# Kernel tuning notes

Measured on AMD Instinct MI355X. Metric: run time of the kernel, lower is better.

## Reference

```python
import jax, jax.numpy as jnp
import numpy as np

KUP = 5       # reassembly kernel size
DELTA = 2     # upsample ratio
KENC = 3      # encoder conv kernel size
CM = 64       # compressed channels
INC = 256
OUTC = 256


def conv2d(x, w, b, pad):
    # x: (N,C,H,W), w: (O,I,kh,kw)
    y = jax.lax.conv_general_dilated(
        x, w, window_strides=(1, 1), padding=[(pad, pad), (pad, pad)],
        dimension_numbers=("NCHW", "OIHW", "NCHW"))
    return y + b[None, :, None, None]


def pixel_shuffle(x, r):
    # torch semantics: channel c*r^2 + i*r + j -> (c, h*r+i, w*r+j)
    N, Cr2, H, W = x.shape
    C = Cr2 // (r * r)
    x = x.reshape(N, C, r, r, H, W)
    x = x.transpose(0, 1, 4, 2, 5, 3)
    return x.reshape(N, C, H * r, W * r)


def setup_inputs() -> dict:
    key = jax.random.key(0)
    ks = jax.random.split(key, 7)
    N, H, W = 4, 64, 64
    x = jax.random.normal(ks[0], (N, INC, H, W), dtype=jnp.float32)
    w_down = jax.random.normal(ks[1], (CM, INC, 1, 1), dtype=jnp.float32) * 0.05
    b_down = jnp.zeros((CM,), jnp.float32)
    enc_out = DELTA * DELTA * KUP * KUP  # 100
    w_enc = jax.random.normal(ks[2], (enc_out, CM, KENC, KENC), dtype=jnp.float32) * 0.05
    b_enc = jnp.zeros((enc_out,), jnp.float32)
    w_out = jax.random.normal(ks[3], (OUTC, INC, 1, 1), dtype=jnp.float32) * 0.05
    b_out = jnp.zeros((OUTC,), jnp.float32)
    return {"in_tensor": x, "w_down": w_down, "b_down": b_down,
            "w_enc": w_enc, "b_enc": b_enc, "w_out": w_out, "b_out": b_out}


def reference(in_tensor, w_down, b_down, w_enc, b_enc, w_out, b_out):
    N, C, H, W = in_tensor.shape
    k2, d2 = KUP * KUP, DELTA * DELTA

    # --- kernel prediction branch ---
    k = conv2d(in_tensor, w_down, b_down, 0)          # (N, Cm, H, W)
    k = conv2d(k, w_enc, b_enc, KENC // 2)            # (N, k2*d2, H, W)
    # pixel_shuffle + per-upsampled-pixel softmax over Kup^2, fused:
    # channel index = kup_idx * delta^2 + subpixel_idx (torch pixel_shuffle layout)
    k = k.reshape(N, k2, d2, H, W)
    k = jax.nn.softmax(k, axis=1)
    kern = k.transpose(0, 3, 4, 1, 2)                 # (N, H, W, k2, d2)

    # --- feature reassembly ---
    pad = KUP // 2
    xp = jnp.pad(in_tensor, ((0, 0), (0, 0), (pad, pad), (pad, pad)))
    # (N, C, H, W, Kup^2); k index = kh*Kup + kw, matching torch unfold order
    patches = jnp.stack(
        [xp[:, :, i:i + H, j:j + W] for i in range(KUP) for j in range(KUP)],
        axis=-1)

    out = jnp.einsum("nchwk,nhwkd->nhwcd", patches, kern)  # (N,H,W,C,d2)
    out = out.reshape(N, H, W, C * d2).transpose(0, 3, 1, 2)  # (N, C*d2, H, W)
    out = pixel_shuffle(out, DELTA)                   # (N, C, H*delta, W*delta)

    return conv2d(out, w_out, b_out, 0)               # (N, outC, H*delta, W*delta)
```

## Files before the change

kernel.cpp:

```cpp
#include <hip/hip_runtime.h>
#include <hip/hip_bf16.h>


namespace {
constexpr int kN = 4, kH = 64, kW = 64, kINC = 256, kCM = 64;
constexpr int kENC = 100, kH2 = 128, kW2 = 128, kOUTC = 256;
constexpr int kHW = kH * kW;
constexpr int kHW2 = kH2 * kW2;
constexpr int kPadW = 66;
constexpr int kTImg = kPadW * kPadW * kCM;
constexpr int kZPad = 68;
constexpr int kZImg = kZPad * kZPad * kOUTC;
}

typedef __attribute__((ext_vector_type(8))) short short8;
typedef __attribute__((ext_vector_type(4))) float floatx4;

static __device__ __forceinline__ unsigned short bf16bits(float f) {
  __hip_bfloat16 h = __float2bfloat16(f);
  return *(unsigned short*)&h;
}

__global__ __launch_bounds__(256) void k_repack(
    const float* __restrict__ we, unsigned short* __restrict__ Aswz) {
  const int e = blockIdx.x * 256 + threadIdx.x;
  if (e >= 9 * 7 * 2 * 512) return;
  const int j = e & 7, lane = (e >> 3) & 63, kh = (e >> 9) & 1, tm = e >> 10;
  const int mt = tm % 7, tap = tm / 7;
  const int o = mt * 16 + (lane & 15);
  const int ci = kh * 32 + ((lane >> 4) & 3) * 8 + j;
  const float v = (o < kENC) ? we[(size_t)o * 576 + ci * 9 + tap] : 0.f;
  Aswz[e] = bf16bits(v);
}

__global__ __launch_bounds__(256) void k_repack_woz(
    const float* __restrict__ wd, const float* __restrict__ wo,
    unsigned short* __restrict__ Awoz) {
  const int e = blockIdx.x * 256 + threadIdx.x;
  if (e >= 8 * 20 * 512) return;
  const int j = e & 7, lane = (e >> 3) & 63;
  const int rest = e >> 9;
  const int mt = rest % 20, ks = rest / 20;
  const int r = mt * 16 + (lane & 15);
  const int k = ks * 32 + (lane >> 4) * 8 + j;
  const float v = (r < kCM) ? wd[(size_t)r * kINC + k]
                            : wo[(size_t)(r - kCM) * kINC + k];
  Awoz[e] = bf16bits(v);
}

__global__ __launch_bounds__(256) void k_dzmfma(
    const float* __restrict__ x, const unsigned short* __restrict__ Awoz,
    const float* __restrict__ bd, __hip_bfloat16* __restrict__ downT,
    float* __restrict__ zT) {
  const int b = blockIdx.x;
  const int pt = b & 255, n = b >> 8;
  const int wave = threadIdx.x >> 6, lane = threadIdx.x & 63;
  const int col = lane & 15, quad = lane >> 4;
  const int px = pt * 16 + col;
  const int h = px >> 6, w = px & 63;
  const float* xb = x + (size_t)n * kINC * kHW + px;

  floatx4 acc[5];
#pragma unroll
  for (int m = 0; m < 5; ++m) acc[m] = (floatx4){0.f, 0.f, 0.f, 0.f};

#pragma unroll
  for (int ks = 0; ks < 8; ++ks) {
    float xv[8];
#pragma unroll
    for (int j = 0; j < 8; ++j)
      xv[j] = xb[(size_t)(ks * 32 + quad * 8 + j) * kHW];
    short8 bf;
#pragma unroll
    for (int j = 0; j < 8; ++j) bf[j] = (short)bf16bits(xv[j]);
#pragma unroll
    for (int m = 0; m < 5; ++m) {
      const int wtile = wave * 5 + m;
      const short8 af = *(const short8*)(
          Awoz + ((size_t)(ks * 20 + wtile) * 64 + lane) * 8);
      acc[m] = __builtin_amdgcn_mfma_f32_16x16x32_bf16(af, bf, acc[m], 0, 0, 0);
    }
  }

#pragma unroll
  for (int m = 0; m < 5; ++m) {
    const int wtile = wave * 5 + m;
    const int r0 = wtile * 16 + quad * 4;
    if (wtile < 4) {
      union { unsigned short u[4]; uint2 v; } pk;
#pragma unroll
      for (int rr = 0; rr < 4; ++rr)
        pk.u[rr] = bf16bits(acc[m][rr] + bd[r0 + rr]);
      __hip_bfloat16* dst = downT + (size_t)n * kTImg
                            + ((h + 1) * kPadW + (w + 1)) * kCM + r0;
      *(uint2*)dst = pk.v;
    } else {
      const int o = r0 - kCM;
      float* dst = zT + (size_t)n * kZImg
                   + ((h + 2) * kZPad + (w + 2)) * kOUTC + o;
      *(float4*)dst = make_float4(acc[m][0], acc[m][1], acc[m][2], acc[m][3]);
    }
  }
}

__global__ __launch_bounds__(256) void k_encmfma(
    const __hip_bfloat16* __restrict__ downT,
    const unsigned short* __restrict__ Aswz,
    const float* __restrict__ be, float* __restrict__ enc) {
  const int b = blockIdx.x;
  const int h = b & 63, mtp = (b >> 6) & 3, n = b >> 8;
  const int wave = threadIdx.x >> 6, lane = threadIdx.x & 63;
  const int w0 = wave << 4;
  const int col = lane & 15, quad = lane >> 4;
  const int mt0 = mtp * 2;
  const bool has2 = (mt0 + 1) < 7;
  const short* dT = (const short*)downT + (size_t)n * kTImg;
  floatx4 acc0 = {0.f, 0.f, 0.f, 0.f}, acc1 = {0.f, 0.f, 0.f, 0.f};
#pragma unroll
  for (int tap = 0; tap < 9; ++tap) {
    const int dh = tap / 3 - 1, dw = tap % 3 - 1;
    const int rowbase = ((h + 1 + dh) * kPadW + (w0 + col + 1 + dw)) * kCM
                        + quad * 8;
#pragma unroll
    for (int kh = 0; kh < 2; ++kh) {
      const short8 bf = *(const short8*)(dT + rowbase + kh * 32);
      const short8 a0 = *(const short8*)(
          Aswz + (((size_t)(tap * 7 + mt0) * 2 + kh) * 64 + lane) * 8);
      acc0 = __builtin_amdgcn_mfma_f32_16x16x32_bf16(a0, bf, acc0, 0, 0, 0);
      if (has2) {
        const short8 a1 = *(const short8*)(
            Aswz + (((size_t)(tap * 7 + mt0 + 1) * 2 + kh) * 64 + lane) * 8);
        acc1 = __builtin_amdgcn_mfma_f32_16x16x32_bf16(a1, bf, acc1, 0, 0, 0);
      }
    }
  }
  const int p = h * kW + w0 + col;
#pragma unroll
  for (int r = 0; r < 4; ++r) {
    const int o = mt0 * 16 + quad * 4 + r;
    if (o < kENC) enc[(size_t)(n * kENC + o) * kHW + p] = acc0[r] + be[o];
  }
  if (has2) {
#pragma unroll
    for (int r = 0; r < 4; ++r) {
      const int o = (mt0 + 1) * 16 + quad * 4 + r;
      if (o < kENC) enc[(size_t)(n * kENC + o) * kHW + p] = acc1[r] + be[o];
    }
  }
}

__global__ __launch_bounds__(64) void k_softmaxT(
    const float* __restrict__ enc, float* __restrict__ kernT) {
  const int t = blockIdx.x * 64 + threadIdx.x;
  const int n = t >> 12, px = t & 4095;
  const float* base = enc + (size_t)n * kENC * kHW + px;
  float v[100];
#pragma unroll
  for (int ch = 0; ch < 100; ++ch) v[ch] = base[(size_t)ch * kHW];
  float inv[4];
#pragma unroll
  for (int d = 0; d < 4; ++d) {
    float m = -1e30f;
#pragma unroll
    for (int k = 0; k < 25; ++k) m = fmaxf(m, v[k * 4 + d]);
    float s = 0.f;
#pragma unroll
    for (int k = 0; k < 25; ++k) { v[k * 4 + d] = __expf(v[k * 4 + d] - m); s += v[k * 4 + d]; }
    inv[d] = 1.f / s;
  }
  float* dst = kernT + ((size_t)n * kHW + px) * 100;
#pragma unroll
  for (int k = 0; k < 25; ++k)
    *(float4*)(dst + k * 4) = make_float4(v[k * 4 + 0] * inv[0], v[k * 4 + 1] * inv[1],
                                          v[k * 4 + 2] * inv[2], v[k * 4 + 3] * inv[3]);
}

__global__ __launch_bounds__(256) void k_fused_out(
    const float* __restrict__ zT, const float* __restrict__ kernT,
    const float* __restrict__ bo, float* __restrict__ out) {
  const int b = blockIdx.x;
  const int pt = b & 255, ob = (b >> 8) & 3, n = b >> 10;
  const int wave = threadIdx.x >> 6, lane = threadIdx.x & 63;
  const int oc = lane & 15, pxi = lane >> 4;
  const int px = pt * 16 + wave * 4 + pxi;
  const int h = px >> 6, w = px & 63;
  const int o = ob * 64 + oc * 4;
  const float* kb = kernT + ((size_t)n * kHW + px) * 100;
  const float* zb = zT + (size_t)n * kZImg + o;
  float acc[4][4] = {};
#pragma unroll
  for (int tap = 0; tap < 25; ++tap) {
    const int kh = tap / 5 - 2, kw = tap % 5 - 2;
    const float4 kf = *(const float4*)(kb + tap * 4);
    const float4 zf = *(const float4*)(
        zb + ((size_t)(h + 2 + kh) * kZPad + (w + 2 + kw)) * kOUTC);
    acc[0][0] += zf.x * kf.x; acc[0][1] += zf.x * kf.y; acc[0][2] += zf.x * kf.z; acc[0][3] += zf.x * kf.w;
    acc[1][0] += zf.y * kf.x; acc[1][1] += zf.y * kf.y; acc[1][2] += zf.y * kf.z; acc[1][3] += zf.y * kf.w;
    acc[2][0] += zf.z * kf.x; acc[2][1] += zf.z * kf.y; acc[2][2] += zf.z * kf.z; acc[2][3] += zf.z * kf.w;
    acc[3][0] += zf.w * kf.x; acc[3][1] += zf.w * kf.y; acc[3][2] += zf.w * kf.z; acc[3][3] += zf.w * kf.w;
  }
#pragma unroll
  for (int oi = 0; oi < 4; ++oi) {
    const float bias = bo[o + oi];
#pragma unroll
    for (int i = 0; i < 2; ++i) {
      float* dst = out + ((size_t)(n * kOUTC + o + oi) * kH2 + (2 * h + i)) * kW2 + 2 * w;
      *(float2*)dst = make_float2(acc[oi][i * 2] + bias, acc[oi][i * 2 + 1] + bias);
    }
  }
}

extern "C" void kernel_launch(void* const* d_in, const int* in_sizes, int n_in,
                              void* d_out, int out_size, void* d_ws, size_t ws_size,
                              hipStream_t stream) {
  const float* x  = (const float*)d_in[0];
  const float* wd = (const float*)d_in[1];
  const float* bd = (const float*)d_in[2];
  const float* we = (const float*)d_in[3];
  const float* be = (const float*)d_in[4];
  const float* wo = (const float*)d_in[5];
  const float* bo = (const float*)d_in[6];
  float* out = (float*)d_out;

  float* enc   = (float*)d_ws;
  float* kernT = enc + 1638400;
  float* zT    = kernT + 1638400;
  __hip_bfloat16* downT = (__hip_bfloat16*)(zT + 4734976);
  unsigned short* Aswz  = (unsigned short*)(downT + (size_t)kN * kTImg);
  unsigned short* Awoz  = Aswz + 64512;

  hipMemsetAsync(downT, 0, (size_t)kN * kTImg * sizeof(__hip_bfloat16), stream);
  hipMemsetAsync(zT, 0, (size_t)kN * kZImg * sizeof(float), stream);
  k_repack<<<252, 256, 0, stream>>>(we, Aswz);
  k_repack_woz<<<320, 256, 0, stream>>>(wd, wo, Awoz);
  k_dzmfma<<<1024, 256, 0, stream>>>(x, Awoz, bd, downT, zT);
  k_encmfma<<<1024, 256, 0, stream>>>(downT, Aswz, be, enc);
  k_softmaxT<<<256, 64, 0, stream>>>(enc, kernT);
  k_fused_out<<<4096, 256, 0, stream>>>(zT, kernT, bo, out);
}
```

Before: 171.0 us.

## Zero only halos, softmax in place, stage kernels in LDS, coalesce output stores

```diff
diff --git a/kernel.cpp b/kernel.cpp
--- a/kernel.cpp
+++ b/kernel.cpp
@@ -19,6 +19,30 @@
 static __device__ __forceinline__ unsigned short bf16bits(float f) {
   __hip_bfloat16 h = __float2bfloat16(f);
   return *(unsigned short*)&h;
+}
+
+__global__ __launch_bounds__(256) void k_halo(
+    float* __restrict__ zT, __hip_bfloat16* __restrict__ downT) {
+  const int t = blockIdx.x * 256 + threadIdx.x;
+  if (t < 4 * 528 * 16) {
+    const int chunk = t & 15, rest = t >> 4;
+    const int i = rest % 528, n = rest / 528;
+    int r, c;
+    if (i < 272) { r = i / 68; if (r >= 2) r += 64; c = i % 68; }
+    else { const int j = i - 272; r = 2 + (j >> 2); const int cc = j & 3; c = (cc < 2) ? cc : cc + 64; }
+    float4* p = (float4*)(zT + (size_t)n * kZImg + ((size_t)r * kZPad + c) * kOUTC) + chunk;
+    *p = make_float4(0.f, 0.f, 0.f, 0.f);
+  } else if (t < 4 * 528 * 16 + 4 * 260 * 8) {
+    const int u = t - 4 * 528 * 16;
+    const int chunk = u & 7, rest = u >> 3;
+    const int i = rest % 260, n = rest / 260;
+    int r, c;
+    if (i < 132) { r = (i / 66) ? 65 : 0; c = i % 66; }
+    else { const int j = i - 132; r = 1 + (j >> 1); c = (j & 1) ? 65 : 0; }
+    float4* p = (float4*)((char*)downT
+                + ((size_t)n * kTImg + ((size_t)r * kPadW + c) * kCM) * 2) + chunk;
+    *p = make_float4(0.f, 0.f, 0.f, 0.f);
+  }
 }
 
 __global__ __launch_bounds__(256) void k_repack(
@@ -149,63 +173,91 @@
   }
 }
 
-__global__ __launch_bounds__(64) void k_softmaxT(
-    const float* __restrict__ enc, float* __restrict__ kernT) {
-  const int t = blockIdx.x * 64 + threadIdx.x;
-  const int n = t >> 12, px = t & 4095;
-  const float* base = enc + (size_t)n * kENC * kHW + px;
-  float v[100];
-#pragma unroll
-  for (int ch = 0; ch < 100; ++ch) v[ch] = base[(size_t)ch * kHW];
-  float inv[4];
-#pragma unroll
-  for (int d = 0; d < 4; ++d) {
-    float m = -1e30f;
-#pragma unroll
-    for (int k = 0; k < 25; ++k) m = fmaxf(m, v[k * 4 + d]);
-    float s = 0.f;
-#pragma unroll
-    for (int k = 0; k < 25; ++k) { v[k * 4 + d] = __expf(v[k * 4 + d] - m); s += v[k * 4 + d]; }
-    inv[d] = 1.f / s;
-  }
-  float* dst = kernT + ((size_t)n * kHW + px) * 100;
-#pragma unroll
-  for (int k = 0; k < 25; ++k)
-    *(float4*)(dst + k * 4) = make_float4(v[k * 4 + 0] * inv[0], v[k * 4 + 1] * inv[1],
-                                          v[k * 4 + 2] * inv[2], v[k * 4 + 3] * inv[3]);
+__global__ __launch_bounds__(256) void k_softmax(float* __restrict__ buf) {
+  const int b = blockIdx.x;
+  const int hg = b & 15, d = (b >> 4) & 3, n = b >> 6;
+  const int tid = threadIdx.x;
+  const int h = (hg << 2) + (tid >> 6), w = tid & 63;
+  float* base = buf + ((size_t)n * kENC + d) * kHW + h * kW + w;
+  float v[25];
+  float m = -1e30f;
+#pragma unroll
+  for (int k = 0; k < 25; ++k) { v[k] = base[(size_t)k * 4 * kHW]; m = fmaxf(m, v[k]); }
+  float s = 0.f;
+#pragma unroll
+  for (int k = 0; k < 25; ++k) { v[k] = __expf(v[k] - m); s += v[k]; }
+  const float inv = 1.f / s;
+#pragma unroll
+  for (int k = 0; k < 25; ++k) base[(size_t)k * 4 * kHW] = v[k] * inv;
 }
 
 __global__ __launch_bounds__(256) void k_fused_out(
-    const float* __restrict__ zT, const float* __restrict__ kernT,
+    const float* __restrict__ zT, const float* __restrict__ enc,
     const float* __restrict__ bo, float* __restrict__ out) {
   const int b = blockIdx.x;
-  const int pt = b & 255, ob = (b >> 8) & 3, n = b >> 10;
-  const int wave = threadIdx.x >> 6, lane = threadIdx.x & 63;
+  const int pt = b & 255, og = (b >> 8) & 3, n = b >> 10;
+  const int tid = threadIdx.x;
+  const int wave = tid >> 6, lane = tid & 63;
+  const int h = pt >> 2, w0 = (pt & 3) << 4;
+  const int px0 = pt * 16;
+
+  __shared__ float lds[64 * 65];
+  float* kernLDS = lds;
+
+  {
+    const int p = tid & 15, chb = tid >> 4;
+#pragma unroll
+    for (int r = 0; r < 7; ++r) {
+      const int ch = r * 16 + chb;
+      if (ch < kENC)
+        kernLDS[p * 104 + ch] = enc[((size_t)n * kENC + ch) * kHW + px0 + p];
+    }
+  }
+  __syncthreads();
+
   const int oc = lane & 15, pxi = lane >> 4;
-  const int px = pt * 16 + wave * 4 + pxi;
-  const int h = px >> 6, w = px & 63;
-  const int o = ob * 64 + oc * 4;
-  const float* kb = kernT + ((size_t)n * kHW + px) * 100;
-  const float* zb = zT + (size_t)n * kZImg + o;
+  const int px_l = wave * 4 + pxi;
+  const int w = w0 + px_l;
+  const int o_l = oc * 4;
+  const float* zb = zT + (size_t)n * kZImg + og * 64 + o_l;
+  const float* kp = kernLDS + px_l * 104;
   float acc[4][4] = {};
 #pragma unroll
   for (int tap = 0; tap < 25; ++tap) {
-    const int kh = tap / 5 - 2, kw = tap % 5 - 2;
-    const float4 kf = *(const float4*)(kb + tap * 4);
+    const int kh = tap / 5, kw = tap % 5;
     const float4 zf = *(const float4*)(
-        zb + ((size_t)(h + 2 + kh) * kZPad + (w + 2 + kw)) * kOUTC);
+        zb + ((size_t)(h + kh) * kZPad + (w + kw)) * kOUTC);
+    const float4 kf = *(const float4*)(kp + tap * 4);
     acc[0][0] += zf.x * kf.x; acc[0][1] += zf.x * kf.y; acc[0][2] += zf.x * kf.z; acc[0][3] += zf.x * kf.w;
     acc[1][0] += zf.y * kf.x; acc[1][1] += zf.y * kf.y; acc[1][2] += zf.y * kf.z; acc[1][3] += zf.y * kf.w;
     acc[2][0] += zf.z * kf.x; acc[2][1] += zf.z * kf.y; acc[2][2] += zf.z * kf.z; acc[2][3] += zf.z * kf.w;
     acc[3][0] += zf.w * kf.x; acc[3][1] += zf.w * kf.y; acc[3][2] += zf.w * kf.z; acc[3][3] += zf.w * kf.w;
   }
-#pragma unroll
-  for (int oi = 0; oi < 4; ++oi) {
-    const float bias = bo[o + oi];
-#pragma unroll
-    for (int i = 0; i < 2; ++i) {
-      float* dst = out + ((size_t)(n * kOUTC + o + oi) * kH2 + (2 * h + i)) * kW2 + 2 * w;
-      *(float2*)dst = make_float2(acc[oi][i * 2] + bias, acc[oi][i * 2 + 1] + bias);
+
+  __syncthreads();
+#pragma unroll
+  for (int oi = 0; oi < 4; ++oi)
+#pragma unroll
+    for (int d = 0; d < 4; ++d)
+      lds[(o_l + oi) * 65 + px_l * 4 + d] = acc[oi][d];
+  __syncthreads();
+
+  const int ol2 = tid >> 2, q = tid & 3;
+  const int o = og * 64 + ol2;
+  const float bias = bo[o];
+  const float* Trow = lds + ol2 * 65;
+#pragma unroll
+  for (int i = 0; i < 2; ++i) {
+    float* row = out + ((size_t)(n * kOUTC + o) * kH2 + (2 * h + i)) * kW2 + 2 * w0;
+#pragma unroll
+    for (int s = 0; s < 2; ++s) {
+      const int xb_ = s * 16 + q * 4;
+      float4 v;
+      v.x = Trow[((xb_ + 0) >> 1) * 4 + i * 2 + ((xb_ + 0) & 1)] + bias;
+      v.y = Trow[((xb_ + 1) >> 1) * 4 + i * 2 + ((xb_ + 1) & 1)] + bias;
+      v.z = Trow[((xb_ + 2) >> 1) * 4 + i * 2 + ((xb_ + 2) & 1)] + bias;
+      v.w = Trow[((xb_ + 3) >> 1) * 4 + i * 2 + ((xb_ + 3) & 1)] + bias;
+      *(float4*)(row + xb_) = v;
     }
   }
 }
@@ -222,19 +274,17 @@
   const float* bo = (const float*)d_in[6];
   float* out = (float*)d_out;
 
-  float* enc   = (float*)d_ws;
-  float* kernT = enc + 1638400;
-  float* zT    = kernT + 1638400;
+  float* enc = (float*)d_ws;
+  float* zT  = enc + 1638400;
   __hip_bfloat16* downT = (__hip_bfloat16*)(zT + 4734976);
   unsigned short* Aswz  = (unsigned short*)(downT + (size_t)kN * kTImg);
   unsigned short* Awoz  = Aswz + 64512;
 
-  hipMemsetAsync(downT, 0, (size_t)kN * kTImg * sizeof(__hip_bfloat16), stream);
-  hipMemsetAsync(zT, 0, (size_t)kN * kZImg * sizeof(float), stream);
+  k_halo<<<165, 256, 0, stream>>>(zT, downT);
   k_repack<<<252, 256, 0, stream>>>(we, Aswz);
   k_repack_woz<<<320, 256, 0, stream>>>(wd, wo, Awoz);
   k_dzmfma<<<1024, 256, 0, stream>>>(x, Awoz, bd, downT, zT);
   k_encmfma<<<1024, 256, 0, stream>>>(downT, Aswz, be, enc);
-  k_softmaxT<<<256, 64, 0, stream>>>(enc, kernT);
-  k_fused_out<<<4096, 256, 0, stream>>>(zT, kernT, bo, out);
-}
+  k_softmax<<<256, 256, 0, stream>>>(enc);
+  k_fused_out<<<4096, 256, 0, stream>>>(zT, enc, bo, out);
+}
```

Result: faster. 150.0 us (-12.3%).
